# Optimization experiments

Hardware: AMD Instinct MI355X
Metric: run time of the kernel (lower is better)

The kernel has to match this reference:

```python
import jax, jax.numpy as jnp
import numpy as np

B, D0, D1, D2, P = 16, 2048, 4096, 4096, 64


def setup_inputs() -> dict:
    key = jax.random.key(0)
    ks = jax.random.split(key, 24)
    n = lambda k, s: jax.random.normal(k, s, dtype=jnp.float32)
    u = lambda k, s: jax.random.uniform(k, s, dtype=jnp.float32)
    return {
        'mu0': n(ks[0], (B, D0, P)),
        'lb1': n(ks[1], (B, D1)), 'ub1': n(ks[2], (B, D1)),
        'lb2': n(ks[3], (B, D2)), 'ub2': n(ks[4], (B, D2)),
        'ps1': n(ks[5], (B, D1)), 'ss1': n(ks[6], (B, D1)),
        'ps2': n(ks[7], (B, D2)), 'ss2': n(ks[8], (B, D2)),
        'mask1': u(ks[9], (B, D1)), 'mask2': u(ks[10], (B, D2)),
        'W1': n(ks[11], (D1, D0)) * 0.02, 'b1': n(ks[12], (D1,)),
        'W2': n(ks[13], (D2, D1)) * 0.02, 'b2': n(ks[14], (D2,)),
        'fc1_W': n(ks[15], (P, 5)) * 0.3, 'fc1_b': n(ks[16], (P,)) * 0.1,
        'fc11_W': n(ks[17], (P, P)) * 0.1, 'fc11_b': n(ks[18], (P,)) * 0.1,
        'fc2_W': n(ks[19], (P, 2 * P)) * 0.1, 'fc2_b': n(ks[20], (P,)) * 0.1,
        'fc21_W': n(ks[21], (P, P)) * 0.1, 'fc21_b': n(ks[22], (P,)) * 0.1,
    }


def compute_ratio(lower, upper):
    # lower - relu(lower) == min(lower, 0); relu(upper) == max(upper, 0)
    lower_temp = jnp.minimum(lower, 0.0)
    upper_temp = jnp.maximum(upper, 0.0)
    diff = upper_temp - lower_temp
    upper_ratio = upper_temp / (diff + 1e-8)
    lower_ratio = 1.0 - upper_ratio
    return upper_ratio, lower_ratio, diff


def _relu_block(pre_flat, lb, ub, ps, ss, mask,
                fc1_W, fc1_b, fc11_W, fc11_b, fc2_W, fc2_b, fc21_W, fc21_b):
    # pre_flat: [N, P] propagated neighbor embeddings; N = B * d_out
    ur, lr, diff = compute_ratio(lb.reshape(-1), ub.reshape(-1))
    info = jnp.stack([ur, lr, diff, ps.reshape(-1), ss.reshape(-1)], axis=-1)  # [N, 5]
    h = jax.nn.relu(info @ fc1_W.T + fc1_b) @ fc11_W.T + fc11_b               # [N, P]
    e = jnp.concatenate([pre_flat, h], axis=-1)                               # [N, 2P]
    out = jax.nn.relu(e @ fc2_W.T + fc2_b) @ fc21_W.T + fc21_b                # [N, P]
    return out * mask.reshape(-1, 1)


def reference(mu0, lb1, ub1, lb2, ub2, ps1, ss1, ps2, ss2, mask1, mask2,
              W1, b1, W2, b2, fc1_W, fc1_b, fc11_W, fc11_b,
              fc2_W, fc2_b, fc21_W, fc21_b):
    # Linear layer 1: W1 @ mu0 + bias (bias broadcast over embedding dim p)
    pre1 = jnp.einsum('oi,bip->bop', W1, mu0) + b1[None, :, None]  # [B, D1, P]
    mu1 = _relu_block(pre1.reshape(-1, P), lb1, ub1, ps1, ss1, mask1,
                      fc1_W, fc1_b, fc11_W, fc11_b, fc2_W, fc2_b, fc21_W, fc21_b)
    mu1 = mu1.reshape(B, D1, P)
    # Linear layer 2
    pre2 = jnp.einsum('oi,bip->bop', W2, mu1) + b2[None, :, None]  # [B, D2, P]
    mu2 = _relu_block(pre2.reshape(-1, P), lb2, ub2, ps2, ss2, mask2,
                      fc1_W, fc1_b, fc11_W, fc11_b, fc2_W, fc2_b, fc21_W, fc21_b)
    mu2 = mu2.reshape(B, D2, P)
    return jnp.stack([mu1, mu2])  # [2, B, D, P] updated embeddings
```

## Files before the change

### kernel.cpp

```cpp
#include <hip/hip_runtime.h>
#include <hip/hip_bf16.h>


#define DOUT 4096
typedef __bf16 bf16x8 __attribute__((ext_vector_type(8)));
typedef float  f32x4  __attribute__((ext_vector_type(4)));

__device__ __forceinline__ __bf16 bfc(float x) { return (__bf16)x; }

__device__ __forceinline__ bf16x8 cvt8(const float4 a, const float4 b) {
    bf16x8 r;
    r[0]=bfc(a.x); r[1]=bfc(a.y); r[2]=bfc(a.z); r[3]=bfc(a.w);
    r[4]=bfc(b.x); r[5]=bfc(b.y); r[6]=bfc(b.z); r[7]=bfc(b.w);
    return r;
}

__device__ __forceinline__ int aoff(int r, int c16) {
    return (r << 7) + ((c16 << 4) ^ ((r & 7) << 4));
}

#define WS_MU0 0
#define WS_MU1 (4u << 20)
#define WS_SM  (12u << 20)

#define BAR() asm volatile("s_barrier" ::: "memory")

__global__ __launch_bounds__(256)
void prepass_kernel(const float* __restrict__ mu0, const float* __restrict__ fc11W,
                    const float* __restrict__ fc2W, const float* __restrict__ fc21W,
                    char* __restrict__ ws)
{
    const int blk = blockIdx.x, t = threadIdx.x;
    if (blk < 512) {
        const int b = blk >> 5, kt = blk & 31;
        const int p = t & 63, kc = t >> 6;
        const float* src = mu0 + ((size_t)b * 2048 + kt * 64 + kc * 16) * 64 + p;
        char* tile = ws + WS_MU0 + ((size_t)b * 32 + kt) * 8192;
        float v[16];
        #pragma unroll
        for (int i = 0; i < 16; ++i) v[i] = src[(size_t)i * 64];
        bf16x8 o0, o1;
        #pragma unroll
        for (int i = 0; i < 8; ++i) { o0[i] = bfc(v[i]); o1[i] = bfc(v[8 + i]); }
        const int n = p >> 4, ks = kc >> 1;
        const int l0 = (((kc & 1) * 2) << 4) | (p & 15);
        const int l1 = (((kc & 1) * 2 + 1) << 4) | (p & 15);
        *(bf16x8*)(tile + ks * 4096 + n * 1024 + l0 * 16) = o0;
        *(bf16x8*)(tile + ks * 4096 + n * 1024 + l1 * 16) = o1;
    } else {
        const int idx = (blk - 512) * 256 + t;
        __bf16* dst = (__bf16*)(ws + WS_SM);
        if (idx < 4096)        dst[idx] = bfc(fc11W[idx]);
        else if (idx < 12288)  dst[idx] = bfc(fc2W[idx - 4096]);
        else                   dst[idx] = bfc(fc21W[idx - 12288]);
    }
}

#define LOADA(dst, t_) { const float* s_ = aSrc + (size_t)(t_) * 64;            \
    dst[0] = *(const float4*)s_;       dst[1] = *(const float4*)(s_ + 4);       \
    dst[2] = *(const float4*)(s_ + 8); dst[3] = *(const float4*)(s_ + 12); }

#define LOADB(dst, t_) { const char* bp_ = bW + (size_t)(t_) * 8192 + lane * 16; \
    _Pragma("unroll")                                                            \
    for (int c_ = 0; c_ < 8; ++c_)                                               \
        dst[c_] = *(const bf16x8*)(bp_ + (c_ >> 2) * 4096 + (c_ & 3) * 1024); }

#define MFMAS(Abuf, bset) {                                                      \
    _Pragma("unroll")                                                            \
    for (int ks_ = 0; ks_ < 2; ++ks_) {                                          \
        bf16x8 af_[4];                                                           \
        _Pragma("unroll")                                                        \
        for (int m_ = 0; m_ < 4; ++m_)                                           \
            af_[m_] = *(const bf16x8*)((Abuf) + aoff(m_ * 16 + lr, ks_ * 4 + lg)); \
        _Pragma("unroll")                                                        \
        for (int m_ = 0; m_ < 4; ++m_)                                           \
            _Pragma("unroll")                                                    \
            for (int n_ = 0; n_ < 4; ++n_)                                       \
                acc[m_][n_] = __builtin_amdgcn_mfma_f32_16x16x32_bf16(           \
                    af_[m_], bset[ks_ * 4 + n_], acc[m_][n_], 0, 0, 0);          \
    } }

template <int K, bool WRITE_T>
__global__ __launch_bounds__(256, 1)
void layer_kernel(const float* __restrict__ W, const float* __restrict__ bias,
                  const char* __restrict__ wsB,
                  const float* __restrict__ lb, const float* __restrict__ ub,
                  const float* __restrict__ ps, const float* __restrict__ ss,
                  const float* __restrict__ mask,
                  const float* __restrict__ fc1W, const float* __restrict__ fc1b,
                  const __bf16* __restrict__ fc11bf, const float* __restrict__ fc11b,
                  const __bf16* __restrict__ fc2bf, const float* __restrict__ fc2b,
                  const __bf16* __restrict__ fc21bf, const float* __restrict__ fc21b,
                  float* __restrict__ out, char* __restrict__ wsT)
{
    constexpr int NT = K / 64;
    __shared__ __align__(16) char lds[65536];
    char* const T_lds = lds;
    char* const hold  = lds + 16384;
    char* const preE  = lds + 32768;
    char* const H_lds = lds + 49152;

    const int tid = threadIdx.x;
    const int lane = tid & 63, wv = tid >> 6;
    const int lr = lane & 15, lg = lane >> 4;

    const int id = blockIdx.x;
    const int xcd = id & 7, lp = id >> 3;
    const int panel = xcd * 8 + (lp & 7);
    const int bgroup = lp >> 3;
    const int orow0 = panel * 64;

    const int batch = bgroup * 4 + wv;
    const char* bW = wsB + (size_t)batch * NT * 8192;

    const int arow = tid >> 2, aslot = tid & 3;
    const float* aSrc = W + (size_t)(orow0 + arow) * K + aslot * 16;
    const int aw0 = aoff(arow, aslot * 2);
    const int aw1 = aoff(arow, aslot * 2 + 1);
    char* const ab0 = lds;
    char* const ab1 = lds + 8192;

    const f32x4 z = {0.f, 0.f, 0.f, 0.f};
    f32x4 acc[4][4];
    #pragma unroll
    for (int m = 0; m < 4; ++m)
        #pragma unroll
        for (int n = 0; n < 4; ++n) acc[m][n] = z;

    float4 aR0[4], aR1[4];
    bf16x8 bR0[8], bR1[8];

    LOADA(aR0, 0); LOADA(aR1, 1);
    LOADB(bR0, 0); LOADB(bR1, 1);
    asm volatile("s_waitcnt vmcnt(8)" ::: "memory");
    *(bf16x8*)(ab0 + aw0) = cvt8(aR0[0], aR0[1]);
    *(bf16x8*)(ab0 + aw1) = cvt8(aR0[2], aR0[3]);
    asm volatile("s_waitcnt lgkmcnt(0)" ::: "memory");
    BAR();

    for (int t = 0; t < NT; t += 2) {
        if (t + 2 < NT) LOADA(aR0, t + 2);
        MFMAS(ab0, bR0);
        if (t + 2 < NT) LOADB(bR0, t + 2);
        if (t + 2 < NT) asm volatile("s_waitcnt vmcnt(12)" ::: "memory");
        else            asm volatile("s_waitcnt vmcnt(0)" ::: "memory");
        *(bf16x8*)(ab1 + aw0) = cvt8(aR1[0], aR1[1]);
        *(bf16x8*)(ab1 + aw1) = cvt8(aR1[2], aR1[3]);
        asm volatile("s_waitcnt lgkmcnt(0)" ::: "memory");
        BAR();
        if (t + 3 < NT) LOADA(aR1, t + 3);
        MFMAS(ab1, bR1);
        if (t + 3 < NT) LOADB(bR1, t + 3);
        if (t + 3 < NT) asm volatile("s_waitcnt vmcnt(12)" ::: "memory");
        else            asm volatile("s_waitcnt vmcnt(0)" ::: "memory");
        if (t + 2 < NT) {
            *(bf16x8*)(ab0 + aw0) = cvt8(aR0[0], aR0[1]);
            *(bf16x8*)(ab0 + aw1) = cvt8(aR0[2], aR0[3]);
        }
        asm volatile("s_waitcnt lgkmcnt(0)" ::: "memory");
        BAR();
    }
    __syncthreads();

    {
        char* dst = (wv < 2) ? (preE + wv * 8192) : (hold + (wv - 2) * 8192);
        #pragma unroll
        for (int m = 0; m < 4; ++m)
            #pragma unroll
            for (int n = 0; n < 4; ++n) {
                const int col = n * 16 + lr;
                #pragma unroll
                for (int r = 0; r < 4; ++r) {
                    const int row = m * 16 + lg * 4 + r;
                    const float bs = bias[orow0 + row];
                    *(__bf16*)(dst + row * 128 + ((2 * col) ^ ((row & 7) << 4))) =
                        bfc(acc[m][n][r] + bs);
                }
            }
    }
    __syncthreads();

    const int wm = wv >> 1, wn = wv & 1;
    #pragma unroll
    for (int p = 0; p < 2; ++p) {
        char* const preB = (p == 0) ? preE : hold;

        {
            const int row = tid >> 1;
            const int j0 = (tid & 1) * 32;
            const int bb = bgroup * 4 + p * 2 + (row >> 6);
            const int g = bb * DOUT + orow0 + (row & 63);
            const float lv = lb[g], uv = ub[g];
            const float lt = fminf(lv, 0.f), ut = fmaxf(uv, 0.f);
            const float diff = ut - lt;
            const float urr = ut / (diff + 1e-8f);
            const float lrr = 1.f - urr, i3 = ps[g], i4 = ss[g];
            #pragma unroll
            for (int c = 0; c < 4; ++c) {
                bf16x8 v;
                #pragma unroll
                for (int jj = 0; jj < 8; ++jj) {
                    const int j = j0 + c * 8 + jj;
                    const float* w = fc1W + j * 5;
                    const float tv = fc1b[j] + urr * w[0] + lrr * w[1] + diff * w[2]
                                   + i3 * w[3] + i4 * w[4];
                    v[jj] = bfc(fmaxf(tv, 0.f));
                }
                *(bf16x8*)(T_lds + aoff(row, (j0 >> 3) + c)) = v;
            }
        }
        __syncthreads();

        {
            f32x4 hacc[4][2];
            #pragma unroll
            for (int m = 0; m < 4; ++m) { hacc[m][0] = z; hacc[m][1] = z; }
            #pragma unroll
            for (int ks = 0; ks < 2; ++ks) {
                bf16x8 a[4];
                #pragma unroll
                for (int m = 0; m < 4; ++m)
                    a[m] = *(const bf16x8*)(T_lds + aoff(wm * 64 + m * 16 + lr, ks * 4 + lg));
                #pragma unroll
                for (int n = 0; n < 2; ++n) {
                    const int j = wn * 32 + n * 16 + lr;
                    const bf16x8 bw = *(const bf16x8*)(fc11bf + (size_t)j * 64 + ks * 32 + lg * 8);
                    #pragma unroll
                    for (int m = 0; m < 4; ++m)
                        hacc[m][n] = __builtin_amdgcn_mfma_f32_16x16x32_bf16(a[m], bw, hacc[m][n], 0, 0, 0);
                }
            }
            char* const Hq = H_lds + wm * 8192;
            #pragma unroll
            for (int n = 0; n < 2; ++n) {
                const int j = wn * 32 + n * 16 + lr;
                const float bj = fc11b[j];
                #pragma unroll
                for (int m = 0; m < 4; ++m)
                    #pragma unroll
                    for (int r = 0; r < 4; ++r) {
                        const int row = m * 16 + lg * 4 + r;
                        *(__bf16*)(Hq + row * 128 + ((2 * j) ^ ((row & 7) << 4))) =
                            bfc(hacc[m][n][r] + bj);
                    }
            }
        }
        __syncthreads();

        {
            f32x4 uacc[4][2];
            #pragma unroll
            for (int m = 0; m < 4; ++m) { uacc[m][0] = z; uacc[m][1] = z; }
            #pragma unroll
            for (int ks = 0; ks < 4; ++ks) {
                const char* base = ((ks < 2) ? preB : H_lds) + wm * 8192;
                const int kb = ((ks & 1) * 64 + lg * 16);
                bf16x8 a[4];
                #pragma unroll
                for (int m = 0; m < 4; ++m) {
                    const int row = m * 16 + lr;
                    a[m] = *(const bf16x8*)(base + row * 128 + (kb ^ ((row & 7) << 4)));
                }
                #pragma unroll
                for (int n = 0; n < 2; ++n) {
                    const int j = wn * 32 + n * 16 + lr;
                    const bf16x8 bw = *(const bf16x8*)(fc2bf + (size_t)j * 128 + ks * 32 + lg * 8);
                    #pragma unroll
                    for (int m = 0; m < 4; ++m)
                        uacc[m][n] = __builtin_amdgcn_mfma_f32_16x16x32_bf16(a[m], bw, uacc[m][n], 0, 0, 0);
                }
            }
            __syncthreads();
            #pragma unroll
            for (int n = 0; n < 2; ++n) {
                const int j = wn * 32 + n * 16 + lr;
                const float bj = fc2b[j];
                #pragma unroll
                for (int m = 0; m < 4; ++m)
                    #pragma unroll
                    for (int r = 0; r < 4; ++r) {
                        const int row = wm * 64 + m * 16 + lg * 4 + r;
                        *(__bf16*)(T_lds + row * 128 + ((2 * j) ^ ((row & 7) << 4))) =
                            bfc(fmaxf(uacc[m][n][r] + bj, 0.f));
                    }
            }
        }
        __syncthreads();

        {
            f32x4 oacc[4][2];
            #pragma unroll
            for (int m = 0; m < 4; ++m) { oacc[m][0] = z; oacc[m][1] = z; }
            #pragma unroll
            for (int ks = 0; ks < 2; ++ks) {
                bf16x8 a[4];
                #pragma unroll
                for (int m = 0; m < 4; ++m)
                    a[m] = *(const bf16x8*)(T_lds + aoff(wm * 64 + m * 16 + lr, ks * 4 + lg));
                #pragma unroll
                for (int n = 0; n < 2; ++n) {
                    const int j = wn * 32 + n * 16 + lr;
                    const bf16x8 bw = *(const bf16x8*)(fc21bf + (size_t)j * 64 + ks * 32 + lg * 8);
                    #pragma unroll
                    for (int m = 0; m < 4; ++m)
                        oacc[m][n] = __builtin_amdgcn_mfma_f32_16x16x32_bf16(a[m], bw, oacc[m][n], 0, 0, 0);
                }
            }
            const int bb = bgroup * 4 + p * 2 + wm;
            #pragma unroll
            for (int n = 0; n < 2; ++n) {
                const int j = wn * 32 + n * 16 + lr;
                const float bj = fc21b[j];
                #pragma unroll
                for (int m = 0; m < 4; ++m)
                    #pragma unroll
                    for (int r = 0; r < 4; ++r) {
                        const int row = m * 16 + lg * 4 + r;
                        const int g = bb * DOUT + orow0 + row;
                        const float o = (oacc[m][n][r] + bj) * mask[g];
                        out[(size_t)g * 64 + j] = o;
                        if (WRITE_T)
                            *(__bf16*)(preE + wm * 8192 + j * 128 +
                                       ((2 * row) ^ ((j & 7) << 4))) = bfc(o);
                    }
            }
        }
        if (WRITE_T) {
            __syncthreads();
            #pragma unroll
            for (int i = 0; i < 4; ++i) {
                const int idx = i * 256 + tid;
                const int qq = idx >> 9, rr = idx & 511;
                const int ks = rr >> 8, n = (rr >> 6) & 3, ln = rr & 63;
                const int j = n * 16 + (ln & 15);
                const int k = ks * 32 + (ln >> 4) * 8;
                const bf16x8 v = *(const bf16x8*)(preE + qq * 8192 + j * 128 +
                                                  ((2 * k) ^ ((j & 7) << 4)));
                const int bb = bgroup * 4 + p * 2 + qq;
                *(bf16x8*)(wsT + ((size_t)bb * 64 + panel) * 8192 +
                           ks * 4096 + n * 1024 + ln * 16) = v;
            }
        }
        __syncthreads();
    }
}

extern "C" void kernel_launch(void* const* d_in, const int* in_sizes, int n_in,
                              void* d_out, int out_size, void* d_ws, size_t ws_size,
                              hipStream_t stream) {
    const float* mu0   = (const float*)d_in[0];
    const float* lb1   = (const float*)d_in[1];
    const float* ub1   = (const float*)d_in[2];
    const float* lb2   = (const float*)d_in[3];
    const float* ub2   = (const float*)d_in[4];
    const float* ps1   = (const float*)d_in[5];
    const float* ss1   = (const float*)d_in[6];
    const float* ps2   = (const float*)d_in[7];
    const float* ss2   = (const float*)d_in[8];
    const float* mask1 = (const float*)d_in[9];
    const float* mask2 = (const float*)d_in[10];
    const float* W1    = (const float*)d_in[11];
    const float* b1    = (const float*)d_in[12];
    const float* W2    = (const float*)d_in[13];
    const float* b2    = (const float*)d_in[14];
    const float* fc1W  = (const float*)d_in[15];
    const float* fc1b  = (const float*)d_in[16];
    const float* fc11W = (const float*)d_in[17];
    const float* fc11b = (const float*)d_in[18];
    const float* fc2W  = (const float*)d_in[19];
    const float* fc2b  = (const float*)d_in[20];
    const float* fc21W = (const float*)d_in[21];
    const float* fc21b = (const float*)d_in[22];

    char* ws = (char*)d_ws;
    float* mu1 = (float*)d_out;
    float* mu2 = (float*)d_out + (size_t)16 * 4096 * 64;
    const __bf16* fc11bf = (const __bf16*)(ws + WS_SM);
    const __bf16* fc2bf  = (const __bf16*)(ws + WS_SM) + 4096;
    const __bf16* fc21bf = (const __bf16*)(ws + WS_SM) + 12288;

    prepass_kernel<<<576, 256, 0, stream>>>(mu0, fc11W, fc2W, fc21W, ws);

    layer_kernel<2048, true><<<256, 256, 0, stream>>>(
        W1, b1, ws + WS_MU0, lb1, ub1, ps1, ss1, mask1,
        fc1W, fc1b, fc11bf, fc11b, fc2bf, fc2b, fc21bf, fc21b,
        mu1, ws + WS_MU1);

    layer_kernel<4096, false><<<256, 256, 0, stream>>>(
        W2, b2, ws + WS_MU1, lb2, ub2, ps2, ss2, mask2,
        fc1W, fc1b, fc11bf, fc11b, fc2bf, fc2b, fc21bf, fc21b,
        mu2, nullptr);
}
```

Measured before the change: 126.0 us.

## Split K across wave pairs, halve batches per block, double grid size

Each block now covers 2 batches instead of 4, and the grid doubles to 512 blocks. Within a block, the four waves form two K-halves times two batches, and the two K-halves' partial accumulators are reduced through LDS. LDS usage drops to 48KB, launch bounds allow 2 blocks per CU, and MFMA issue is wrapped in s_setprio. This aims to raise occupancy and the number of blocks in flight so latency is better hidden. The cost is that every W tile is loaded and converted twice as often across blocks, plus an extra LDS reduction step.

```diff
diff --git a/kernel.cpp b/kernel.cpp
--- a/kernel.cpp
+++ b/kernel.cpp
@@ -62,26 +62,24 @@
 
 #define LOADB(dst, t_) { const char* bp_ = bW + (size_t)(t_) * 8192 + lane * 16; \
     _Pragma("unroll")                                                            \
-    for (int c_ = 0; c_ < 8; ++c_)                                               \
-        dst[c_] = *(const bf16x8*)(bp_ + (c_ >> 2) * 4096 + (c_ & 3) * 1024); }
+    for (int n_ = 0; n_ < 4; ++n_) dst[n_] = *(const bf16x8*)(bp_ + n_ * 1024); }
 
 #define MFMAS(Abuf, bset) {                                                      \
+    bf16x8 af_[4];                                                               \
     _Pragma("unroll")                                                            \
-    for (int ks_ = 0; ks_ < 2; ++ks_) {                                          \
-        bf16x8 af_[4];                                                           \
+    for (int m_ = 0; m_ < 4; ++m_)                                               \
+        af_[m_] = *(const bf16x8*)((Abuf) + aoff(m_ * 16 + lr, khc + lg));       \
+    __builtin_amdgcn_s_setprio(1);                                               \
+    _Pragma("unroll")                                                            \
+    for (int m_ = 0; m_ < 4; ++m_)                                               \
         _Pragma("unroll")                                                        \
-        for (int m_ = 0; m_ < 4; ++m_)                                           \
-            af_[m_] = *(const bf16x8*)((Abuf) + aoff(m_ * 16 + lr, ks_ * 4 + lg)); \
-        _Pragma("unroll")                                                        \
-        for (int m_ = 0; m_ < 4; ++m_)                                           \
-            _Pragma("unroll")                                                    \
-            for (int n_ = 0; n_ < 4; ++n_)                                       \
-                acc[m_][n_] = __builtin_amdgcn_mfma_f32_16x16x32_bf16(           \
-                    af_[m_], bset[ks_ * 4 + n_], acc[m_][n_], 0, 0, 0);          \
-    } }
+        for (int n_ = 0; n_ < 4; ++n_)                                           \
+            acc[m_][n_] = __builtin_amdgcn_mfma_f32_16x16x32_bf16(               \
+                af_[m_], bset[n_], acc[m_][n_], 0, 0, 0);                        \
+    __builtin_amdgcn_s_setprio(0); }
 
 template <int K, bool WRITE_T>
-__global__ __launch_bounds__(256, 1)
+__global__ __launch_bounds__(256, 2)
 void layer_kernel(const float* __restrict__ W, const float* __restrict__ bias,
                   const char* __restrict__ wsB,
                   const float* __restrict__ lb, const float* __restrict__ ub,
@@ -94,24 +92,25 @@
                   float* __restrict__ out, char* __restrict__ wsT)
 {
     constexpr int NT = K / 64;
-    __shared__ __align__(16) char lds[65536];
+    __shared__ __align__(16) char lds[49152];
+    char* const pre   = lds + 32768;
     char* const T_lds = lds;
-    char* const hold  = lds + 16384;
-    char* const preE  = lds + 32768;
-    char* const H_lds = lds + 49152;
+    char* const H_lds = lds + 16384;
 
     const int tid = threadIdx.x;
     const int lane = tid & 63, wv = tid >> 6;
+    const int kh = wv >> 1, bn = wv & 1;
+    const int khc = kh * 4;
     const int lr = lane & 15, lg = lane >> 4;
 
     const int id = blockIdx.x;
-    const int xcd = id & 7, lp = id >> 3;
-    const int panel = xcd * 8 + (lp & 7);
-    const int bgroup = lp >> 3;
+    const int vid = (id & 7) * 64 + (id >> 3);
+    const int panel = vid >> 3;
+    const int bgroup = vid & 7;
     const int orow0 = panel * 64;
-
-    const int batch = bgroup * 4 + wv;
-    const char* bW = wsB + (size_t)batch * NT * 8192;
+    const int batch0 = bgroup * 2;
+
+    const char* bW = wsB + ((size_t)(batch0 + bn) * NT) * 8192 + khc * 1024;
 
     const int arow = tid >> 2, aslot = tid & 3;
     const float* aSrc = W + (size_t)(orow0 + arow) * K + aslot * 16;
@@ -128,10 +127,10 @@
         for (int n = 0; n < 4; ++n) acc[m][n] = z;
 
     float4 aR0[4], aR1[4];
-    bf16x8 bR0[8], bR1[8];
-
-    LOADA(aR0, 0); LOADA(aR1, 1);
-    LOADB(bR0, 0); LOADB(bR1, 1);
+    bf16x8 bR0[4], bR1[4];
+
+    LOADA(aR0, 0); LOADB(bR0, 0);
+    LOADA(aR1, 1); LOADB(bR1, 1);
     asm volatile("s_waitcnt vmcnt(8)" ::: "memory");
     *(bf16x8*)(ab0 + aw0) = cvt8(aR0[0], aR0[1]);
     *(bf16x8*)(ab0 + aw1) = cvt8(aR0[2], aR0[3]);
@@ -142,7 +141,7 @@
         if (t + 2 < NT) LOADA(aR0, t + 2);
         MFMAS(ab0, bR0);
         if (t + 2 < NT) LOADB(bR0, t + 2);
-        if (t + 2 < NT) asm volatile("s_waitcnt vmcnt(12)" ::: "memory");
+        if (t + 2 < NT) asm volatile("s_waitcnt vmcnt(8)" ::: "memory");
         else            asm volatile("s_waitcnt vmcnt(0)" ::: "memory");
         *(bf16x8*)(ab1 + aw0) = cvt8(aR1[0], aR1[1]);
         *(bf16x8*)(ab1 + aw1) = cvt8(aR1[2], aR1[3]);
@@ -151,7 +150,7 @@
         if (t + 3 < NT) LOADA(aR1, t + 3);
         MFMAS(ab1, bR1);
         if (t + 3 < NT) LOADB(bR1, t + 3);
-        if (t + 3 < NT) asm volatile("s_waitcnt vmcnt(12)" ::: "memory");
+        if (t + 3 < NT) asm volatile("s_waitcnt vmcnt(8)" ::: "memory");
         else            asm volatile("s_waitcnt vmcnt(0)" ::: "memory");
         if (t + 2 < NT) {
             *(bf16x8*)(ab0 + aw0) = cvt8(aR0[0], aR0[1]);
@@ -162,8 +161,21 @@
     }
     __syncthreads();
 
-    {
-        char* dst = (wv < 2) ? (preE + wv * 8192) : (hold + (wv - 2) * 8192);
+    if (kh == 0) {
+        #pragma unroll
+        for (int m = 0; m < 4; ++m)
+            #pragma unroll
+            for (int n = 0; n < 4; ++n)
+                *(f32x4*)(lds + bn * 16384 + ((m * 4 + n) * 64 + lane) * 16) = acc[m][n];
+    }
+    __syncthreads();
+    if (kh == 1) {
+        #pragma unroll
+        for (int m = 0; m < 4; ++m)
+            #pragma unroll
+            for (int n = 0; n < 4; ++n)
+                acc[m][n] += *(const f32x4*)(lds + bn * 16384 + ((m * 4 + n) * 64 + lane) * 16);
+        char* const dst = pre + bn * 8192;
         #pragma unroll
         for (int m = 0; m < 4; ++m)
             #pragma unroll
@@ -181,167 +193,162 @@
     __syncthreads();
 
     const int wm = wv >> 1, wn = wv & 1;
-    #pragma unroll
-    for (int p = 0; p < 2; ++p) {
-        char* const preB = (p == 0) ? preE : hold;
-
-        {
-            const int row = tid >> 1;
-            const int j0 = (tid & 1) * 32;
-            const int bb = bgroup * 4 + p * 2 + (row >> 6);
-            const int g = bb * DOUT + orow0 + (row & 63);
-            const float lv = lb[g], uv = ub[g];
-            const float lt = fminf(lv, 0.f), ut = fmaxf(uv, 0.f);
-            const float diff = ut - lt;
-            const float urr = ut / (diff + 1e-8f);
-            const float lrr = 1.f - urr, i3 = ps[g], i4 = ss[g];
-            #pragma unroll
-            for (int c = 0; c < 4; ++c) {
-                bf16x8 v;
-                #pragma unroll
-                for (int jj = 0; jj < 8; ++jj) {
-                    const int j = j0 + c * 8 + jj;
-                    const float* w = fc1W + j * 5;
-                    const float tv = fc1b[j] + urr * w[0] + lrr * w[1] + diff * w[2]
-                                   + i3 * w[3] + i4 * w[4];
-                    v[jj] = bfc(fmaxf(tv, 0.f));
-                }
-                *(bf16x8*)(T_lds + aoff(row, (j0 >> 3) + c)) = v;
-            }
-        }
-        __syncthreads();
-
-        {
-            f32x4 hacc[4][2];
-            #pragma unroll
-            for (int m = 0; m < 4; ++m) { hacc[m][0] = z; hacc[m][1] = z; }
-            #pragma unroll
-            for (int ks = 0; ks < 2; ++ks) {
-                bf16x8 a[4];
-                #pragma unroll
-                for (int m = 0; m < 4; ++m)
-                    a[m] = *(const bf16x8*)(T_lds + aoff(wm * 64 + m * 16 + lr, ks * 4 + lg));
-                #pragma unroll
-                for (int n = 0; n < 2; ++n) {
-                    const int j = wn * 32 + n * 16 + lr;
-                    const bf16x8 bw = *(const bf16x8*)(fc11bf + (size_t)j * 64 + ks * 32 + lg * 8);
-                    #pragma unroll
-                    for (int m = 0; m < 4; ++m)
-                        hacc[m][n] = __builtin_amdgcn_mfma_f32_16x16x32_bf16(a[m], bw, hacc[m][n], 0, 0, 0);
-                }
-            }
-            char* const Hq = H_lds + wm * 8192;
+
+    {
+        const int row = tid >> 1;
+        const int j0 = (tid & 1) * 32;
+        const int bb = batch0 + (row >> 6);
+        const int g = bb * DOUT + orow0 + (row & 63);
+        const float lv = lb[g], uv = ub[g];
+        const float lt = fminf(lv, 0.f), ut = fmaxf(uv, 0.f);
+        const float diff = ut - lt;
+        const float urr = ut / (diff + 1e-8f);
+        const float lrr = 1.f - urr, i3 = ps[g], i4 = ss[g];
+        #pragma unroll
+        for (int c = 0; c < 4; ++c) {
+            bf16x8 v;
+            #pragma unroll
+            for (int jj = 0; jj < 8; ++jj) {
+                const int j = j0 + c * 8 + jj;
+                const float* w = fc1W + j * 5;
+                const float tv = fc1b[j] + urr * w[0] + lrr * w[1] + diff * w[2]
+                               + i3 * w[3] + i4 * w[4];
+                v[jj] = bfc(fmaxf(tv, 0.f));
+            }
+            *(bf16x8*)(T_lds + aoff(row, (j0 >> 3) + c)) = v;
+        }
+    }
+    __syncthreads();
+
+    {
+        f32x4 hacc[4][2];
+        #pragma unroll
+        for (int m = 0; m < 4; ++m) { hacc[m][0] = z; hacc[m][1] = z; }
+        #pragma unroll
+        for (int ks = 0; ks < 2; ++ks) {
+            bf16x8 a[4];
+            #pragma unroll
+            for (int m = 0; m < 4; ++m)
+                a[m] = *(const bf16x8*)(T_lds + aoff(wm * 64 + m * 16 + lr, ks * 4 + lg));
             #pragma unroll
             for (int n = 0; n < 2; ++n) {
                 const int j = wn * 32 + n * 16 + lr;
-                const float bj = fc11b[j];
+                const bf16x8 bw = *(const bf16x8*)(fc11bf + (size_t)j * 64 + ks * 32 + lg * 8);
                 #pragma unroll
                 for (int m = 0; m < 4; ++m)
-                    #pragma unroll
-                    for (int r = 0; r < 4; ++r) {
-                        const int row = m * 16 + lg * 4 + r;
-                        *(__bf16*)(Hq + row * 128 + ((2 * j) ^ ((row & 7) << 4))) =
-                            bfc(hacc[m][n][r] + bj);
-                    }
-            }
-        }
-        __syncthreads();
-
-        {
-            f32x4 uacc[4][2];
-            #pragma unroll
-            for (int m = 0; m < 4; ++m) { uacc[m][0] = z; uacc[m][1] = z; }
-            #pragma unroll
-            for (int ks = 0; ks < 4; ++ks) {
-                const char* base = ((ks < 2) ? preB : H_lds) + wm * 8192;
-                const int kb = ((ks & 1) * 64 + lg * 16);
-                bf16x8 a[4];
-                #pragma unroll
-                for (int m = 0; m < 4; ++m) {
-                    const int row = m * 16 + lr;
-                    a[m] = *(const bf16x8*)(base + row * 128 + (kb ^ ((row & 7) << 4)));
+                    hacc[m][n] = __builtin_amdgcn_mfma_f32_16x16x32_bf16(a[m], bw, hacc[m][n], 0, 0, 0);
+            }
+        }
+        char* const Hq = H_lds + wm * 8192;
+        #pragma unroll
+        for (int n = 0; n < 2; ++n) {
+            const int j = wn * 32 + n * 16 + lr;
+            const float bj = fc11b[j];
+            #pragma unroll
+            for (int m = 0; m < 4; ++m)
+                #pragma unroll
+                for (int r = 0; r < 4; ++r) {
+                    const int row = m * 16 + lg * 4 + r;
+                    *(__bf16*)(Hq + row * 128 + ((2 * j) ^ ((row & 7) << 4))) =
+                        bfc(hacc[m][n][r] + bj);
                 }
-                #pragma unroll
-                for (int n = 0; n < 2; ++n) {
-                    const int j = wn * 32 + n * 16 + lr;
-                    const bf16x8 bw = *(const bf16x8*)(fc2bf + (size_t)j * 128 + ks * 32 + lg * 8);
-                    #pragma unroll
-                    for (int m = 0; m < 4; ++m)
-                        uacc[m][n] = __builtin_amdgcn_mfma_f32_16x16x32_bf16(a[m], bw, uacc[m][n], 0, 0, 0);
-                }
-            }
-            __syncthreads();
+        }
+    }
+    __syncthreads();
+
+    {
+        f32x4 uacc[4][2];
+        #pragma unroll
+        for (int m = 0; m < 4; ++m) { uacc[m][0] = z; uacc[m][1] = z; }
+        #pragma unroll
+        for (int ks = 0; ks < 4; ++ks) {
+            const char* base = ((ks < 2) ? pre : H_lds) + wm * 8192;
+            const int kb = ((ks & 1) * 64 + lg * 16);
+            bf16x8 a[4];
+            #pragma unroll
+            for (int m = 0; m < 4; ++m) {
+                const int row = m * 16 + lr;
+                a[m] = *(const bf16x8*)(base + row * 128 + (kb ^ ((row & 7) << 4)));
+            }
             #pragma unroll
             for (int n = 0; n < 2; ++n) {
                 const int j = wn * 32 + n * 16 + lr;
-                const float bj = fc2b[j];
+                const bf16x8 bw = *(const bf16x8*)(fc2bf + (size_t)j * 128 + ks * 32 + lg * 8);
                 #pragma unroll
                 for (int m = 0; m < 4; ++m)
-                    #pragma unroll
-                    for (int r = 0; r < 4; ++r) {
-                        const int row = wm * 64 + m * 16 + lg * 4 + r;
-                        *(__bf16*)(T_lds + row * 128 + ((2 * j) ^ ((row & 7) << 4))) =
-                            bfc(fmaxf(uacc[m][n][r] + bj, 0.f));
-                    }
+                    uacc[m][n] = __builtin_amdgcn_mfma_f32_16x16x32_bf16(a[m], bw, uacc[m][n], 0, 0, 0);
             }
         }
         __syncthreads();
-
-        {
-            f32x4 oacc[4][2];
-            #pragma unroll
-            for (int m = 0; m < 4; ++m) { oacc[m][0] = z; oacc[m][1] = z; }
-            #pragma unroll
-            for (int ks = 0; ks < 2; ++ks) {
-                bf16x8 a[4];
-                #pragma unroll
-                for (int m = 0; m < 4; ++m)
-                    a[m] = *(const bf16x8*)(T_lds + aoff(wm * 64 + m * 16 + lr, ks * 4 + lg));
-                #pragma unroll
-                for (int n = 0; n < 2; ++n) {
-                    const int j = wn * 32 + n * 16 + lr;
-                    const bf16x8 bw = *(const bf16x8*)(fc21bf + (size_t)j * 64 + ks * 32 + lg * 8);
-                    #pragma unroll
-                    for (int m = 0; m < 4; ++m)
-                        oacc[m][n] = __builtin_amdgcn_mfma_f32_16x16x32_bf16(a[m], bw, oacc[m][n], 0, 0, 0);
+        #pragma unroll
+        for (int n = 0; n < 2; ++n) {
+            const int j = wn * 32 + n * 16 + lr;
+            const float bj = fc2b[j];
+            #pragma unroll
+            for (int m = 0; m < 4; ++m)
+                #pragma unroll
+                for (int r = 0; r < 4; ++r) {
+                    const int row = wm * 64 + m * 16 + lg * 4 + r;
+                    *(__bf16*)(T_lds + row * 128 + ((2 * j) ^ ((row & 7) << 4))) =
+                        bfc(fmaxf(uacc[m][n][r] + bj, 0.f));
                 }
-            }
-            const int bb = bgroup * 4 + p * 2 + wm;
+        }
+    }
+    __syncthreads();
+
+    {
+        f32x4 oacc[4][2];
+        #pragma unroll
+        for (int m = 0; m < 4; ++m) { oacc[m][0] = z; oacc[m][1] = z; }
+        #pragma unroll
+        for (int ks = 0; ks < 2; ++ks) {
+            bf16x8 a[4];
+            #pragma unroll
+            for (int m = 0; m < 4; ++m)
+                a[m] = *(const bf16x8*)(T_lds + aoff(wm * 64 + m * 16 + lr, ks * 4 + lg));
             #pragma unroll
             for (int n = 0; n < 2; ++n) {
                 const int j = wn * 32 + n * 16 + lr;
-                const float bj = fc21b[j];
+                const bf16x8 bw = *(const bf16x8*)(fc21bf + (size_t)j * 64 + ks * 32 + lg * 8);
                 #pragma unroll
                 for (int m = 0; m < 4; ++m)
-                    #pragma unroll
-                    for (int r = 0; r < 4; ++r) {
-                        const int row = m * 16 + lg * 4 + r;
-                        const int g = bb * DOUT + orow0 + row;
-                        const float o = (oacc[m][n][r] + bj) * mask[g];
-                        out[(size_t)g * 64 + j] = o;
-                        if (WRITE_T)
-                            *(__bf16*)(preE + wm * 8192 + j * 128 +
-                                       ((2 * row) ^ ((j & 7) << 4))) = bfc(o);
-                    }
-            }
-        }
-        if (WRITE_T) {
-            __syncthreads();
-            #pragma unroll
-            for (int i = 0; i < 4; ++i) {
-                const int idx = i * 256 + tid;
-                const int qq = idx >> 9, rr = idx & 511;
-                const int ks = rr >> 8, n = (rr >> 6) & 3, ln = rr & 63;
-                const int j = n * 16 + (ln & 15);
-                const int k = ks * 32 + (ln >> 4) * 8;
-                const bf16x8 v = *(const bf16x8*)(preE + qq * 8192 + j * 128 +
-                                                  ((2 * k) ^ ((j & 7) << 4)));
-                const int bb = bgroup * 4 + p * 2 + qq;
-                *(bf16x8*)(wsT + ((size_t)bb * 64 + panel) * 8192 +
-                           ks * 4096 + n * 1024 + ln * 16) = v;
-            }
-        }
+                    oacc[m][n] = __builtin_amdgcn_mfma_f32_16x16x32_bf16(a[m], bw, oacc[m][n], 0, 0, 0);
+            }
+        }
+        const int bb = batch0 + wm;
+        #pragma unroll
+        for (int n = 0; n < 2; ++n) {
+            const int j = wn * 32 + n * 16 + lr;
+            const float bj = fc21b[j];
+            #pragma unroll
+            for (int m = 0; m < 4; ++m)
+                #pragma unroll
+                for (int r = 0; r < 4; ++r) {
+                    const int row = m * 16 + lg * 4 + r;
+                    const int g = bb * DOUT + orow0 + row;
+                    const float o = (oacc[m][n][r] + bj) * mask[g];
+                    out[(size_t)g * 64 + j] = o;
+                    if (WRITE_T)
+                        *(__bf16*)(H_lds + wm * 8192 + j * 128 +
+                                   ((2 * row) ^ ((j & 7) << 4))) = bfc(o);
+                }
+        }
+    }
+    if (WRITE_T) {
         __syncthreads();
+        #pragma unroll
+        for (int i = 0; i < 4; ++i) {
+            const int idx = i * 256 + tid;
+            const int qq = idx >> 9, rr = idx & 511;
+            const int ks = rr >> 8, n = (rr >> 6) & 3, ln = rr & 63;
+            const int j = n * 16 + (ln & 15);
+            const int k = ks * 32 + (ln >> 4) * 8;
+            const bf16x8 v = *(const bf16x8*)(H_lds + qq * 8192 + j * 128 +
+                                              ((2 * k) ^ ((j & 7) << 4)));
+            const int bb = batch0 + qq;
+            *(bf16x8*)(wsT + ((size_t)bb * 64 + panel) * 8192 +
+                       ks * 4096 + n * 1024 + ln * 16) = v;
+        }
     }
 }
 
@@ -381,12 +388,12 @@
 
     prepass_kernel<<<576, 256, 0, stream>>>(mu0, fc11W, fc2W, fc21W, ws);
 
-    layer_kernel<2048, true><<<256, 256, 0, stream>>>(
+    layer_kernel<2048, true><<<512, 256, 0, stream>>>(
         W1, b1, ws + WS_MU0, lb1, ub1, ps1, ss1, mask1,
         fc1W, fc1b, fc11bf, fc11b, fc2bf, fc2b, fc21bf, fc21b,
         mu1, ws + WS_MU1);
 
-    layer_kernel<4096, false><<<256, 256, 0, stream>>>(
+    layer_kernel<4096, false><<<512, 256, 0, stream>>>(
         W2, b2, ws + WS_MU1, lb2, ub2, ps2, ss2, mask2,
         fc1W, fc1b, fc11bf, fc11b, fc2bf, fc2b, fc21bf, fc21b,
         mu2, nullptr);
```

Result: faster. 118.1 us (-6.3%).
